# Kernel tuning notes

Hardware: AMD Instinct MI355X
Metric: run time of the kernel (lower is better)

Reference implementation:

```python
import jax, jax.numpy as jnp
import numpy as np

N_NODES = 100000
N_EDGES = 600000
D_IN = 128
D_OUT = 128


def setup_inputs() -> dict:
    key = jax.random.key(0)
    ks = jax.random.split(key, 8)
    stdv = 1.0 / np.sqrt(D_OUT)
    return {
        "x": jax.random.normal(ks[0], (N_NODES, D_IN), dtype=jnp.float32),
        "edge_src": jax.random.randint(ks[1], (N_EDGES,), 0, N_NODES, dtype=jnp.int32),
        "edge_dst": jax.random.randint(ks[2], (N_EDGES,), 0, N_NODES, dtype=jnp.int32),
        "edge_weight": jax.random.uniform(ks[3], (N_EDGES,), dtype=jnp.float32),
        "weight_l": jax.random.uniform(ks[4], (D_IN, D_OUT), minval=-stdv, maxval=stdv, dtype=jnp.float32),
        "bias_l": jax.random.uniform(ks[5], (D_OUT,), minval=-stdv, maxval=stdv, dtype=jnp.float32),
        "weight_r": jax.random.uniform(ks[6], (D_IN, D_OUT), minval=-stdv, maxval=stdv, dtype=jnp.float32),
        "bias_r": jax.random.uniform(ks[7], (D_OUT,), minval=-stdv, maxval=stdv, dtype=jnp.float32),
    }


def reference(x, edge_src, edge_dst, edge_weight, weight_l, bias_l, weight_r, bias_r):
    # h = input @ weight_l  -> [N, D_OUT]
    h = x @ weight_l
    # spmm(adj, h): out[dst] += adj[dst, src] * h[src]
    msgs = h[edge_src] * edge_weight[:, None]          # [E, D_OUT] gather
    agg = jax.ops.segment_sum(msgs, edge_dst, num_segments=N_NODES)
    out = agg + bias_l
    # root_weight branch (size is None)
    out = out + x @ weight_r + bias_r
    return out
```

## Files before the change

### kernel.cpp

```cpp
#include <hip/hip_runtime.h>
#include <hip/hip_bf16.h>

#define D 128
#define SCAN_BLK 256
#define SCAN_VPT 4
#define SCAN_TILE (SCAN_BLK * SCAN_VPT)

typedef __attribute__((ext_vector_type(8))) short short8;
typedef __attribute__((ext_vector_type(4))) float f32x4;

__global__ __launch_bounds__(256) void prep_w(
    const float* __restrict__ Wl, const float* __restrict__ Wr,
    const float* __restrict__ bl, const float* __restrict__ br,
    __hip_bfloat16* __restrict__ WTl, __hip_bfloat16* __restrict__ WTr,
    float* __restrict__ bsum) {
  const int tid = blockIdx.x * 256 + threadIdx.x;
  const int n = (tid >> 7) & 127;
  const int k = tid & 127;
  if (tid < 16384) {
    WTl[n * D + k] = __float2bfloat16(Wl[k * D + n]);
  } else {
    WTr[n * D + k] = __float2bfloat16(Wr[k * D + n]);
  }
  if (tid < 128) bsum[tid] = bl[tid] + br[tid];
}

__global__ __launch_bounds__(256) void gemm_h(
    const float* __restrict__ x, const __hip_bfloat16* __restrict__ WTl,
    __hip_bfloat16* __restrict__ h,
    const int* __restrict__ edst, int* __restrict__ deg, int n_edges,
    int n_rowtiles) {
  const int gsz = gridDim.x * 256;
  for (int e = blockIdx.x * 256 + threadIdx.x; e < n_edges; e += gsz)
    atomicAdd(&deg[edst[e]], 1);

  __shared__ __hip_bfloat16 xs[16][136];
  const int t = threadIdx.x;
  const int wave = t >> 6;
  const int lane = t & 63;
  const int m = lane & 15;
  const int q = lane >> 4;

  short8 bfrag[2][4];
#pragma unroll
  for (int c = 0; c < 2; ++c) {
    const int n0 = wave * 32 + c * 16;
#pragma unroll
    for (int ks = 0; ks < 4; ++ks)
      bfrag[c][ks] = *(const short8*)&WTl[(n0 + m) * D + ks * 32 + q * 8];
  }

  const int srow = t >> 4;
  const int scol = (t & 15) * 8;

  for (int rt = blockIdx.x; rt < n_rowtiles; rt += gridDim.x) {
    const int rowbase = rt * 16;
    {
      const float4* src = (const float4*)&x[(size_t)(rowbase + srow) * D + scol];
      const float4 v0 = src[0], v1 = src[1];
      __hip_bfloat16* dst = &xs[srow][scol];
      dst[0] = __float2bfloat16(v0.x); dst[1] = __float2bfloat16(v0.y);
      dst[2] = __float2bfloat16(v0.z); dst[3] = __float2bfloat16(v0.w);
      dst[4] = __float2bfloat16(v1.x); dst[5] = __float2bfloat16(v1.y);
      dst[6] = __float2bfloat16(v1.z); dst[7] = __float2bfloat16(v1.w);
    }
    __syncthreads();

    f32x4 acc[2];
#pragma unroll
    for (int c = 0; c < 2; ++c)
#pragma unroll
      for (int r = 0; r < 4; ++r) acc[c][r] = 0.f;

#pragma unroll
    for (int ks = 0; ks < 4; ++ks) {
      const short8 afrag = *(const short8*)&xs[m][ks * 32 + q * 8];
#pragma unroll
      for (int c = 0; c < 2; ++c)
        acc[c] = __builtin_amdgcn_mfma_f32_16x16x32_bf16(afrag, bfrag[c][ks], acc[c], 0, 0, 0);
    }

#pragma unroll
    for (int c = 0; c < 2; ++c) {
      const int n = wave * 32 + c * 16 + m;
#pragma unroll
      for (int r = 0; r < 4; ++r)
        h[(size_t)(rowbase + q * 4 + r) * D + n] = __float2bfloat16(acc[c][r]);
    }
    __syncthreads();
  }
}

__global__ __launch_bounds__(SCAN_BLK) void scan1_kernel(
    const int* __restrict__ deg, int* __restrict__ offsets,
    int* __restrict__ partials, int n) {
  __shared__ int sdata[SCAN_BLK];
  const int t = threadIdx.x;
  const int base = blockIdx.x * SCAN_TILE + t * SCAN_VPT;

  int v[SCAN_VPT];
  int s = 0;
#pragma unroll
  for (int j = 0; j < SCAN_VPT; ++j) {
    v[j] = (base + j < n) ? deg[base + j] : 0;
    s += v[j];
  }
  sdata[t] = s;
  __syncthreads();
  for (int off = 1; off < SCAN_BLK; off <<= 1) {
    int xv = (t >= off) ? sdata[t - off] : 0;
    __syncthreads();
    sdata[t] += xv;
    __syncthreads();
  }
  int excl = sdata[t] - s;
  if (t == SCAN_BLK - 1) partials[blockIdx.x] = sdata[t];
  int run = excl;
#pragma unroll
  for (int j = 0; j < SCAN_VPT; ++j) {
    if (base + j < n) offsets[base + j] = run;
    run += v[j];
  }
}

__global__ __launch_bounds__(SCAN_BLK) void scan3_kernel(
    int* __restrict__ offsets, int* __restrict__ pos,
    const int* __restrict__ partials, int n, int n_edges) {
  __shared__ int s_add;
  const int t = threadIdx.x;
  if (t < 64) {
    int v = 0;
    for (int j = t; j < blockIdx.x; j += 64) v += partials[j];
#pragma unroll
    for (int off = 32; off > 0; off >>= 1) v += __shfl_down(v, off);
    if (t == 0) s_add = v;
  }
  __syncthreads();
  const int add = s_add;
  const int base = blockIdx.x * SCAN_TILE + t * SCAN_VPT;
#pragma unroll
  for (int j = 0; j < SCAN_VPT; ++j) {
    const int i = base + j;
    if (i < n) {
      const int o = offsets[i] + add;
      offsets[i] = o;
      pos[i] = o;
    }
  }
  if (blockIdx.x == 0 && t == 0) offsets[n] = n_edges;
}

__global__ __launch_bounds__(256) void scatter_kernel(
    const int* __restrict__ esrc, const int* __restrict__ edst,
    const float* __restrict__ ew, int* __restrict__ pos,
    int2* __restrict__ pairs, int n_edges) {
  const int e = blockIdx.x * 256 + threadIdx.x;
  if (e >= n_edges) return;
  const int d = edst[e];
  const int slot = atomicAdd(&pos[d], 1);
  pairs[slot] = make_int2(esrc[e], __float_as_int(ew[e]));
}

__global__ __launch_bounds__(256) void sage_out(
    const float* __restrict__ x, const __hip_bfloat16* __restrict__ WTr,
    const float* __restrict__ bsum, const __hip_bfloat16* __restrict__ h,
    const int* __restrict__ offsets, const int2* __restrict__ pairs,
    float* __restrict__ out) {
  __shared__ __hip_bfloat16 xs[16][136];
  __shared__ float ot[16][D];
  const int t = threadIdx.x;
  const int wave = t >> 6;
  const int lane = t & 63;
  const int m = lane & 15;
  const int q = lane >> 4;
  const int rowbase = blockIdx.x * 16;

  short8 bfrag[2][4];
#pragma unroll
  for (int c = 0; c < 2; ++c) {
    const int n0 = wave * 32 + c * 16;
#pragma unroll
    for (int ks = 0; ks < 4; ++ks)
      bfrag[c][ks] = *(const short8*)&WTr[(n0 + m) * D + ks * 32 + q * 8];
  }

  {
    const int srow = t >> 4;
    const int scol = (t & 15) * 8;
    const float4* src = (const float4*)&x[(size_t)(rowbase + srow) * D + scol];
    const float4 v0 = src[0], v1 = src[1];
    __hip_bfloat16* dst = &xs[srow][scol];
    dst[0] = __float2bfloat16(v0.x); dst[1] = __float2bfloat16(v0.y);
    dst[2] = __float2bfloat16(v0.z); dst[3] = __float2bfloat16(v0.w);
    dst[4] = __float2bfloat16(v1.x); dst[5] = __float2bfloat16(v1.y);
    dst[6] = __float2bfloat16(v1.z); dst[7] = __float2bfloat16(v1.w);
  }
  __syncthreads();

  f32x4 acc[2];
#pragma unroll
  for (int c = 0; c < 2; ++c)
#pragma unroll
    for (int r = 0; r < 4; ++r) acc[c][r] = 0.f;

#pragma unroll
  for (int ks = 0; ks < 4; ++ks) {
    const short8 afrag = *(const short8*)&xs[m][ks * 32 + q * 8];
#pragma unroll
    for (int c = 0; c < 2; ++c)
      acc[c] = __builtin_amdgcn_mfma_f32_16x16x32_bf16(afrag, bfrag[c][ks], acc[c], 0, 0, 0);
  }

#pragma unroll
  for (int c = 0; c < 2; ++c) {
    const int n = wave * 32 + c * 16 + m;
    const float b = bsum[n];
#pragma unroll
    for (int r = 0; r < 4; ++r)
      ot[q * 4 + r][n] = acc[c][r] + b;
  }
  __syncthreads();

  const __hip_bfloat162* __restrict__ h2 = (const __hip_bfloat162*)h;
#pragma unroll
  for (int j = 0; j < 4; ++j) {
    const int ln = wave * 4 + j;
    const int node = rowbase + ln;
    const int begin = offsets[node];
    const int end = offsets[node + 1];

    float2 a = *(const float2*)&ot[ln][2 * lane];

    int i = begin;
    for (; i + 4 <= end; i += 4) {
      const int2 p0 = pairs[i + 0];
      const int2 p1 = pairs[i + 1];
      const int2 p2 = pairs[i + 2];
      const int2 p3 = pairs[i + 3];
      const __hip_bfloat162 a0 = h2[(size_t)p0.x * (D / 2) + lane];
      const __hip_bfloat162 a1 = h2[(size_t)p1.x * (D / 2) + lane];
      const __hip_bfloat162 a2 = h2[(size_t)p2.x * (D / 2) + lane];
      const __hip_bfloat162 a3 = h2[(size_t)p3.x * (D / 2) + lane];
      const float w0 = __int_as_float(p0.y), w1 = __int_as_float(p1.y);
      const float w2 = __int_as_float(p2.y), w3 = __int_as_float(p3.y);
      a.x = fmaf(w0, __bfloat162float(a0.x), a.x);
      a.y = fmaf(w0, __bfloat162float(a0.y), a.y);
      a.x = fmaf(w1, __bfloat162float(a1.x), a.x);
      a.y = fmaf(w1, __bfloat162float(a1.y), a.y);
      a.x = fmaf(w2, __bfloat162float(a2.x), a.x);
      a.y = fmaf(w2, __bfloat162float(a2.y), a.y);
      a.x = fmaf(w3, __bfloat162float(a3.x), a.x);
      a.y = fmaf(w3, __bfloat162float(a3.y), a.y);
    }
    for (; i < end; ++i) {
      const int2 p = pairs[i];
      const __hip_bfloat162 av = h2[(size_t)p.x * (D / 2) + lane];
      const float w = __int_as_float(p.y);
      a.x = fmaf(w, __bfloat162float(av.x), a.x);
      a.y = fmaf(w, __bfloat162float(av.y), a.y);
    }
    *(float2*)&out[(size_t)node * D + 2 * lane] = a;
  }
}

extern "C" void kernel_launch(void* const* d_in, const int* in_sizes, int n_in,
                              void* d_out, int out_size, void* d_ws, size_t ws_size,
                              hipStream_t stream) {
  const float* x   = (const float*)d_in[0];
  const int* esrc  = (const int*)d_in[1];
  const int* edst  = (const int*)d_in[2];
  const float* ew  = (const float*)d_in[3];
  const float* Wl  = (const float*)d_in[4];
  const float* bl  = (const float*)d_in[5];
  const float* Wr  = (const float*)d_in[6];
  const float* br  = (const float*)d_in[7];
  float* out = (float*)d_out;

  const int n_nodes = in_sizes[0] / D;
  const int n_edges = in_sizes[1];

  char* ws = (char*)d_ws;
  size_t off = 0;
  __hip_bfloat16* h = (__hip_bfloat16*)(ws + off);
  off += (size_t)n_nodes * D * sizeof(__hip_bfloat16);
  off = (off + 15) & ~15ull;
  int* offsets = (int*)(ws + off);
  off += (size_t)(n_nodes + 1) * sizeof(int);
  off = (off + 15) & ~15ull;
  int* pos = (int*)(ws + off);
  off += (size_t)n_nodes * sizeof(int);
  off = (off + 15) & ~15ull;
  int* partials = (int*)(ws + off);
  off += 1024 * sizeof(int);
  off = (off + 15) & ~15ull;
  int2* pairs = (int2*)(ws + off);
  off += (size_t)n_edges * sizeof(int2);
  off = (off + 15) & ~15ull;
  __hip_bfloat16* WTl = (__hip_bfloat16*)(ws + off);
  off += (size_t)D * D * sizeof(__hip_bfloat16);
  __hip_bfloat16* WTr = (__hip_bfloat16*)(ws + off);
  off += (size_t)D * D * sizeof(__hip_bfloat16);
  float* bsum = (float*)(ws + off);
  off += D * sizeof(float);

  const int n_rowtiles = (n_nodes + 15) / 16;

  hipMemsetAsync(pos, 0, (size_t)n_nodes * sizeof(int), stream);
  prep_w<<<128, 256, 0, stream>>>(Wl, Wr, bl, br, WTl, WTr, bsum);

  const int gemm_grid = n_rowtiles < 2048 ? n_rowtiles : 2048;
  gemm_h<<<gemm_grid, 256, 0, stream>>>(x, WTl, h, edst, pos, n_edges, n_rowtiles);

  const int nparts = (n_nodes + SCAN_TILE - 1) / SCAN_TILE;
  scan1_kernel<<<nparts, SCAN_BLK, 0, stream>>>(pos, offsets, partials, n_nodes);
  scan3_kernel<<<nparts, SCAN_BLK, 0, stream>>>(offsets, pos, partials, n_nodes, n_edges);
  scatter_kernel<<<(n_edges + 255) / 256, 256, 0, stream>>>(esrc, edst, ew, pos, pairs, n_edges);

  sage_out<<<n_rowtiles, 256, 0, stream>>>(x, WTr, bsum, h, offsets, pairs, out);
}
```

Measured before the change: 236.9 us.

## Fuse root-weight GEMM into first GEMM and split aggregation into lightweight kernel

Both x@Wl and x@Wr are now computed in one GEMM pass over x, so x is read and converted once. The root branch plus bias is written straight into out. The aggregation kernel becomes a one-wave-per-node gather that reads out, adds the neighbour contributions and writes it back. That kernel uses an 8-way unrolled, predicated gather so more loads are in flight. The degree memset is folded into prep_w. The cost is an extra fp32 read and write of out, traded against dropping the second x read and the second GEMM.

```diff
diff --git a/kernel.cpp b/kernel.cpp
--- a/kernel.cpp
+++ b/kernel.cpp
@@ -13,7 +13,7 @@
     const float* __restrict__ Wl, const float* __restrict__ Wr,
     const float* __restrict__ bl, const float* __restrict__ br,
     __hip_bfloat16* __restrict__ WTl, __hip_bfloat16* __restrict__ WTr,
-    float* __restrict__ bsum) {
+    float* __restrict__ bsum, int* __restrict__ deg, int n_nodes) {
   const int tid = blockIdx.x * 256 + threadIdx.x;
   const int n = (tid >> 7) & 127;
   const int k = tid & 127;
@@ -23,11 +23,13 @@
     WTr[n * D + k] = __float2bfloat16(Wr[k * D + n]);
   }
   if (tid < 128) bsum[tid] = bl[tid] + br[tid];
-}
-
-__global__ __launch_bounds__(256) void gemm_h(
+  for (int i = tid; i < n_nodes; i += 32768) deg[i] = 0;
+}
+
+__global__ __launch_bounds__(256) void gemm_hr(
     const float* __restrict__ x, const __hip_bfloat16* __restrict__ WTl,
-    __hip_bfloat16* __restrict__ h,
+    const __hip_bfloat16* __restrict__ WTr, const float* __restrict__ bsum,
+    __hip_bfloat16* __restrict__ h, float* __restrict__ out,
     const int* __restrict__ edst, int* __restrict__ deg, int n_edges,
     int n_rowtiles) {
   const int gsz = gridDim.x * 256;
@@ -41,13 +43,17 @@
   const int m = lane & 15;
   const int q = lane >> 4;
 
-  short8 bfrag[2][4];
+  short8 bfl[2][4], bfr[2][4];
+  float bias[2];
 #pragma unroll
   for (int c = 0; c < 2; ++c) {
     const int n0 = wave * 32 + c * 16;
-#pragma unroll
-    for (int ks = 0; ks < 4; ++ks)
-      bfrag[c][ks] = *(const short8*)&WTl[(n0 + m) * D + ks * 32 + q * 8];
+    bias[c] = bsum[n0 + m];
+#pragma unroll
+    for (int ks = 0; ks < 4; ++ks) {
+      bfl[c][ks] = *(const short8*)&WTl[(n0 + m) * D + ks * 32 + q * 8];
+      bfr[c][ks] = *(const short8*)&WTr[(n0 + m) * D + ks * 32 + q * 8];
+    }
   }
 
   const int srow = t >> 4;
@@ -66,26 +72,31 @@
     }
     __syncthreads();
 
-    f32x4 acc[2];
+    f32x4 accL[2], accR[2];
 #pragma unroll
     for (int c = 0; c < 2; ++c)
 #pragma unroll
-      for (int r = 0; r < 4; ++r) acc[c][r] = 0.f;
+      for (int r = 0; r < 4; ++r) { accL[c][r] = 0.f; accR[c][r] = 0.f; }
 
 #pragma unroll
     for (int ks = 0; ks < 4; ++ks) {
       const short8 afrag = *(const short8*)&xs[m][ks * 32 + q * 8];
 #pragma unroll
-      for (int c = 0; c < 2; ++c)
-        acc[c] = __builtin_amdgcn_mfma_f32_16x16x32_bf16(afrag, bfrag[c][ks], acc[c], 0, 0, 0);
+      for (int c = 0; c < 2; ++c) {
+        accL[c] = __builtin_amdgcn_mfma_f32_16x16x32_bf16(afrag, bfl[c][ks], accL[c], 0, 0, 0);
+        accR[c] = __builtin_amdgcn_mfma_f32_16x16x32_bf16(afrag, bfr[c][ks], accR[c], 0, 0, 0);
+      }
     }
 
 #pragma unroll
     for (int c = 0; c < 2; ++c) {
       const int n = wave * 32 + c * 16 + m;
 #pragma unroll
-      for (int r = 0; r < 4; ++r)
-        h[(size_t)(rowbase + q * 4 + r) * D + n] = __float2bfloat16(acc[c][r]);
+      for (int r = 0; r < 4; ++r) {
+        const size_t row = (size_t)(rowbase + q * 4 + r);
+        h[row * D + n] = __float2bfloat16(accL[c][r]);
+        out[row * D + n] = accR[c][r] + bias[c];
+      }
     }
     __syncthreads();
   }
@@ -161,106 +172,56 @@
   pairs[slot] = make_int2(esrc[e], __float_as_int(ew[e]));
 }
 
-__global__ __launch_bounds__(256) void sage_out(
-    const float* __restrict__ x, const __hip_bfloat16* __restrict__ WTr,
-    const float* __restrict__ bsum, const __hip_bfloat16* __restrict__ h,
+__global__ __launch_bounds__(256) void sage_agg(
+    const __hip_bfloat16* __restrict__ h,
     const int* __restrict__ offsets, const int2* __restrict__ pairs,
-    float* __restrict__ out) {
-  __shared__ __hip_bfloat16 xs[16][136];
-  __shared__ float ot[16][D];
-  const int t = threadIdx.x;
-  const int wave = t >> 6;
-  const int lane = t & 63;
-  const int m = lane & 15;
-  const int q = lane >> 4;
-  const int rowbase = blockIdx.x * 16;
-
-  short8 bfrag[2][4];
-#pragma unroll
-  for (int c = 0; c < 2; ++c) {
-    const int n0 = wave * 32 + c * 16;
-#pragma unroll
-    for (int ks = 0; ks < 4; ++ks)
-      bfrag[c][ks] = *(const short8*)&WTr[(n0 + m) * D + ks * 32 + q * 8];
-  }
-
-  {
-    const int srow = t >> 4;
-    const int scol = (t & 15) * 8;
-    const float4* src = (const float4*)&x[(size_t)(rowbase + srow) * D + scol];
-    const float4 v0 = src[0], v1 = src[1];
-    __hip_bfloat16* dst = &xs[srow][scol];
-    dst[0] = __float2bfloat16(v0.x); dst[1] = __float2bfloat16(v0.y);
-    dst[2] = __float2bfloat16(v0.z); dst[3] = __float2bfloat16(v0.w);
-    dst[4] = __float2bfloat16(v1.x); dst[5] = __float2bfloat16(v1.y);
-    dst[6] = __float2bfloat16(v1.z); dst[7] = __float2bfloat16(v1.w);
-  }
-  __syncthreads();
-
-  f32x4 acc[2];
-#pragma unroll
-  for (int c = 0; c < 2; ++c)
-#pragma unroll
-    for (int r = 0; r < 4; ++r) acc[c][r] = 0.f;
-
-#pragma unroll
-  for (int ks = 0; ks < 4; ++ks) {
-    const short8 afrag = *(const short8*)&xs[m][ks * 32 + q * 8];
-#pragma unroll
-    for (int c = 0; c < 2; ++c)
-      acc[c] = __builtin_amdgcn_mfma_f32_16x16x32_bf16(afrag, bfrag[c][ks], acc[c], 0, 0, 0);
-  }
-
-#pragma unroll
-  for (int c = 0; c < 2; ++c) {
-    const int n = wave * 32 + c * 16 + m;
-    const float b = bsum[n];
-#pragma unroll
-    for (int r = 0; r < 4; ++r)
-      ot[q * 4 + r][n] = acc[c][r] + b;
-  }
-  __syncthreads();
-
+    float* __restrict__ out, int n_nodes) {
+  const int node = blockIdx.x * 4 + (threadIdx.x >> 6);
+  const int lane = threadIdx.x & 63;
+  if (node >= n_nodes) return;
+  const int begin = offsets[node];
+  const int end = offsets[node + 1];
   const __hip_bfloat162* __restrict__ h2 = (const __hip_bfloat162*)h;
-#pragma unroll
-  for (int j = 0; j < 4; ++j) {
-    const int ln = wave * 4 + j;
-    const int node = rowbase + ln;
-    const int begin = offsets[node];
-    const int end = offsets[node + 1];
-
-    float2 a = *(const float2*)&ot[ln][2 * lane];
-
-    int i = begin;
-    for (; i + 4 <= end; i += 4) {
-      const int2 p0 = pairs[i + 0];
-      const int2 p1 = pairs[i + 1];
-      const int2 p2 = pairs[i + 2];
-      const int2 p3 = pairs[i + 3];
-      const __hip_bfloat162 a0 = h2[(size_t)p0.x * (D / 2) + lane];
-      const __hip_bfloat162 a1 = h2[(size_t)p1.x * (D / 2) + lane];
-      const __hip_bfloat162 a2 = h2[(size_t)p2.x * (D / 2) + lane];
-      const __hip_bfloat162 a3 = h2[(size_t)p3.x * (D / 2) + lane];
-      const float w0 = __int_as_float(p0.y), w1 = __int_as_float(p1.y);
-      const float w2 = __int_as_float(p2.y), w3 = __int_as_float(p3.y);
-      a.x = fmaf(w0, __bfloat162float(a0.x), a.x);
-      a.y = fmaf(w0, __bfloat162float(a0.y), a.y);
-      a.x = fmaf(w1, __bfloat162float(a1.x), a.x);
-      a.y = fmaf(w1, __bfloat162float(a1.y), a.y);
-      a.x = fmaf(w2, __bfloat162float(a2.x), a.x);
-      a.y = fmaf(w2, __bfloat162float(a2.y), a.y);
-      a.x = fmaf(w3, __bfloat162float(a3.x), a.x);
-      a.y = fmaf(w3, __bfloat162float(a3.y), a.y);
-    }
-    for (; i < end; ++i) {
-      const int2 p = pairs[i];
-      const __hip_bfloat162 av = h2[(size_t)p.x * (D / 2) + lane];
-      const float w = __int_as_float(p.y);
-      a.x = fmaf(w, __bfloat162float(av.x), a.x);
-      a.y = fmaf(w, __bfloat162float(av.y), a.y);
-    }
-    *(float2*)&out[(size_t)node * D + 2 * lane] = a;
-  }
+
+  float2 a = *(const float2*)&out[(size_t)node * D + 2 * lane];
+
+  int i = begin;
+  for (; i + 8 <= end; i += 8) {
+    int2 p[8];
+#pragma unroll
+    for (int u = 0; u < 8; ++u) p[u] = pairs[i + u];
+    __hip_bfloat162 hv[8];
+#pragma unroll
+    for (int u = 0; u < 8; ++u)
+      hv[u] = h2[(size_t)p[u].x * (D / 2) + lane];
+#pragma unroll
+    for (int u = 0; u < 8; ++u) {
+      const float w = __int_as_float(p[u].y);
+      a.x = fmaf(w, __bfloat162float(hv[u].x), a.x);
+      a.y = fmaf(w, __bfloat162float(hv[u].y), a.y);
+    }
+  }
+  if (i < end) {
+    int2 p[8];
+#pragma unroll
+    for (int u = 0; u < 8; ++u) {
+      const int ei = (i + u < end) ? (i + u) : (end - 1);
+      p[u] = pairs[ei];
+      if (i + u >= end) p[u].y = 0;
+    }
+    __hip_bfloat162 hv[8];
+#pragma unroll
+    for (int u = 0; u < 8; ++u)
+      hv[u] = h2[(size_t)p[u].x * (D / 2) + lane];
+#pragma unroll
+    for (int u = 0; u < 8; ++u) {
+      const float w = __int_as_float(p[u].y);
+      a.x = fmaf(w, __bfloat162float(hv[u].x), a.x);
+      a.y = fmaf(w, __bfloat162float(hv[u].y), a.y);
+    }
+  }
+
+  *(float2*)&out[(size_t)node * D + 2 * lane] = a;
 }
 
 extern "C" void kernel_launch(void* const* d_in, const int* in_sizes, int n_in,
@@ -305,16 +266,16 @@
 
   const int n_rowtiles = (n_nodes + 15) / 16;
 
-  hipMemsetAsync(pos, 0, (size_t)n_nodes * sizeof(int), stream);
-  prep_w<<<128, 256, 0, stream>>>(Wl, Wr, bl, br, WTl, WTr, bsum);
+  prep_w<<<128, 256, 0, stream>>>(Wl, Wr, bl, br, WTl, WTr, bsum, pos, n_nodes);
 
   const int gemm_grid = n_rowtiles < 2048 ? n_rowtiles : 2048;
-  gemm_h<<<gemm_grid, 256, 0, stream>>>(x, WTl, h, edst, pos, n_edges, n_rowtiles);
+  gemm_hr<<<gemm_grid, 256, 0, stream>>>(x, WTl, WTr, bsum, h, out, edst, pos,
+                                         n_edges, n_rowtiles);
 
   const int nparts = (n_nodes + SCAN_TILE - 1) / SCAN_TILE;
   scan1_kernel<<<nparts, SCAN_BLK, 0, stream>>>(pos, offsets, partials, n_nodes);
   scan3_kernel<<<nparts, SCAN_BLK, 0, stream>>>(offsets, pos, partials, n_nodes, n_edges);
   scatter_kernel<<<(n_edges + 255) / 256, 256, 0, stream>>>(esrc, edst, ew, pos, pairs, n_edges);
 
-  sage_out<<<n_rowtiles, 256, 0, stream>>>(x, WTr, bsum, h, offsets, pairs, out);
-}
+  sage_agg<<<(n_nodes + 3) / 4, 256, 0, stream>>>(h, offsets, pairs, out, n_nodes);
+}
```

Measured after the change: 236.7 us. About the same (-0.1%).
